# Optimization experiments

Hardware: AMD Instinct MI355X
Metric: run time of the kernel (lower is better)

## Reference

```python
import jax, jax.numpy as jnp
import numpy as np

G, M, H, HEADS, FFN, MAX_DIST, E = 8, 1024, 256, 8, 1024, 5, 131072
N = G * M
HD = H // HEADS

def _ln(x, g, b, eps=1e-5):
    m = x.mean(-1, keepdims=True)
    v = ((x - m) ** 2).mean(-1, keepdims=True)
    return (x - m) / jnp.sqrt(v + eps) * g + b

def _forward(x, gcn_w, gcn_b, qkv_w, qkv_b, proj_w, proj_b,
             ln1_g, ln1_b, ln2_g, ln2_b, ffn1_w, ffn1_b, ffn2_w, ffn2_b,
             bias_emb, oln1_g, oln1_b, oln2_g, oln2_b,
             offn1_w, offn1_b, offn2_w, offn2_b, edge_index, batch):
    src, dst = edge_index[0], edge_index[1]
    # --- local conv: GCNConv (self-loops + symmetric normalization) ---
    sl = jnp.arange(N, dtype=src.dtype)
    s2 = jnp.concatenate([src, sl]); d2 = jnp.concatenate([dst, sl])
    xw = x @ gcn_w.T
    deg = jax.ops.segment_sum(jnp.ones_like(d2, dtype=x.dtype), d2, num_segments=N)
    dinv = jnp.where(deg > 0, 1.0 / jnp.sqrt(deg), 0.0)
    norm = dinv[s2] * dinv[d2]
    x_local = jax.ops.segment_sum(xw[s2] * norm[:, None], d2, num_segments=N) + gcn_b
    # --- to_dense_batch ---
    counts = jax.ops.segment_sum(jnp.ones(N, jnp.int32), batch, num_segments=G)
    starts = jnp.concatenate([jnp.zeros(1, jnp.int32), jnp.cumsum(counts)[:-1]])
    local = jnp.arange(N, dtype=jnp.int32) - starts[batch]
    dense_x = jnp.zeros((G, M, H), x.dtype).at[batch, local].set(x)
    mask = jnp.zeros((G, M), bool).at[batch, local].set(True)
    # --- SPD via batched boolean adjacency powering (== per-node BFS capped at MAX_DIST) ---
    g_e = batch[src]
    valid = (batch[src] == batch[dst]) & (src != dst)
    ls, ld = local[src], local[dst]
    adj = jnp.zeros((G, M, M), bool).at[g_e, ls, ld].max(valid).at[g_e, ld, ls].max(valid)
    dist = jnp.full((G, M, M), MAX_DIST + 1, jnp.int32)
    eye = jnp.eye(M, dtype=bool)[None]
    dist = jnp.where(eye & mask[:, :, None], 0, dist)
    reach = adj
    dist = jnp.where(reach, jnp.minimum(dist, 1), dist)
    for d in range(2, MAX_DIST + 1):
        reach = jnp.einsum('gij,gjk->gik', reach.astype(x.dtype), adj.astype(x.dtype)) > 0
        dist = jnp.where(reach, jnp.minimum(dist, d), dist)
    attn_bias = bias_emb[dist][..., 0]  # [G, M, M]
    # --- Graphormer encoder layer (layers=1) ---
    h = dense_x
    qkv = (h @ qkv_w.T + qkv_b).reshape(G, M, 3, HEADS, HD).transpose(2, 0, 3, 1, 4)
    q, k, v = qkv[0], qkv[1], qkv[2]  # [G, heads, M, hd]
    scores = jnp.einsum('ghqd,ghkd->ghqk', q, k) * (HD ** -0.5)
    scores = scores + attn_bias[:, None].astype(scores.dtype)
    pad = ~mask
    scores = jnp.where(pad[:, None, None, :], -jnp.inf, scores)
    attn = jax.nn.softmax(scores, axis=-1)
    out = jnp.einsum('ghqk,ghkd->ghqd', attn, v).transpose(0, 2, 1, 3).reshape(G, M, H)
    out = out @ proj_w.T + proj_b
    h = _ln(h + out, ln1_g, ln1_b)
    ff = jax.nn.gelu(h @ ffn1_w.T + ffn1_b, approximate=False) @ ffn2_w.T + ffn2_b
    h = _ln(h + ff, ln2_g, ln2_b)
    h = jnp.where(pad[..., None], 0.0, h)
    x_global = h[batch, local]
    # --- GPS combine + outer FFN (dropout = identity at eval) ---
    y = _ln(x + (x_local + x_global), oln1_g, oln1_b)
    ff2 = jax.nn.gelu(y @ offn1_w.T + offn1_b, approximate=False) @ offn2_w.T + offn2_b
    return _ln(y + ff2, oln2_g, oln2_b)

def setup_inputs() -> dict:
    key = jax.random.key(0)
    ks = jax.random.split(key, 16)
    w = lambda k, *s: jax.random.normal(k, s, jnp.float32) * 0.02
    src = jax.random.randint(ks[0], (E,), 0, N, jnp.int32)
    # keep each edge inside one graph (graphs are contiguous blocks of M nodes)
    dst = (src // M) * M + jax.random.randint(ks[1], (E,), 0, M, jnp.int32)
    return dict(
        x=jax.random.normal(ks[2], (N, H), jnp.float32),
        gcn_w=w(ks[3], H, H), gcn_b=jnp.zeros((H,), jnp.float32),
        qkv_w=w(ks[4], 3 * H, H), qkv_b=jnp.zeros((3 * H,), jnp.float32),
        proj_w=w(ks[5], H, H), proj_b=jnp.zeros((H,), jnp.float32),
        ln1_g=jnp.ones((H,), jnp.float32), ln1_b=jnp.zeros((H,), jnp.float32),
        ln2_g=jnp.ones((H,), jnp.float32), ln2_b=jnp.zeros((H,), jnp.float32),
        ffn1_w=w(ks[6], FFN, H), ffn1_b=jnp.zeros((FFN,), jnp.float32),
        ffn2_w=w(ks[7], H, FFN), ffn2_b=jnp.zeros((H,), jnp.float32),
        bias_emb=w(ks[8], MAX_DIST + 2, 1),
        oln1_g=jnp.ones((H,), jnp.float32), oln1_b=jnp.zeros((H,), jnp.float32),
        oln2_g=jnp.ones((H,), jnp.float32), oln2_b=jnp.zeros((H,), jnp.float32),
        offn1_w=w(ks[9], FFN, H), offn1_b=jnp.zeros((FFN,), jnp.float32),
        offn2_w=w(ks[10], H, FFN), offn2_b=jnp.zeros((H,), jnp.float32),
        edge_index=jnp.stack([src, dst]),
        batch=(jnp.arange(N, dtype=jnp.int32) // M),
    )

def reference(x, gcn_w, gcn_b, qkv_w, qkv_b, proj_w, proj_b,
              ln1_g, ln1_b, ln2_g, ln2_b, ffn1_w, ffn1_b, ffn2_w, ffn2_b,
              bias_emb, oln1_g, oln1_b, oln2_g, oln2_b,
              offn1_w, offn1_b, offn2_w, offn2_b, edge_index, batch):
    return _forward(x, gcn_w, gcn_b, qkv_w, qkv_b, proj_w, proj_b,
                    ln1_g, ln1_b, ln2_g, ln2_b, ffn1_w, ffn1_b, ffn2_w, ffn2_b,
                    bias_emb, oln1_g, oln1_b, oln2_g, oln2_b,
                    offn1_w, offn1_b, offn2_w, offn2_b, edge_index, batch)
```

## Files before the change

### kernel.cpp

```cpp
#include <hip/hip_runtime.h>
#include <hip/hip_bf16.h>
#include <cstdint>

#define G 8
#define M 1024
#define H 256
#define HEADS 8
#define FFND 1024
#define NE 131072
#define NN (G*M)
#define HD 32

typedef unsigned long long u64;
typedef uint8_t u8;
typedef unsigned short ushort_t;
typedef __attribute__((ext_vector_type(8))) short bf16x8;
typedef __attribute__((ext_vector_type(4))) float f32x4;

__device__ __forceinline__ short f2b(float v) {
  __hip_bfloat16 h = __float2bfloat16(v);
  return *reinterpret_cast<short*>(&h);
}
__device__ __forceinline__ float b2f(unsigned int u) {
  union { float f; unsigned int i; } v; v.i = u << 16; return v.f;
}

typedef __attribute__((address_space(1))) const void gvoid;
typedef __attribute__((address_space(3))) void lvoid;
__device__ __forceinline__ void gload16(const void* g, void* l) {
  __builtin_amdgcn_global_load_lds((gvoid*)g, (lvoid*)l, 16, 0, 0);
}

__global__ void k_prep(const int* __restrict__ srcv, const int* __restrict__ dstv,
                       int* __restrict__ deg, int* __restrict__ deg2) {
  int e = blockIdx.x * 256 + threadIdx.x;
  if (e >= NE) return;
  int d = dstv[e], s = srcv[e];
  atomicAdd(&deg[d], 1);
  if (s != d) { atomicAdd(&deg2[s], 1); atomicAdd(&deg2[d], 1); }
}

__global__ __launch_bounds__(1024) void k_scan2(const int* __restrict__ deg, const int* __restrict__ deg2,
                                                int* __restrict__ starts, int* __restrict__ starts2,
                                                float* __restrict__ dinv) {
  __shared__ int tmp[1024];
  const int* in = blockIdx.x ? deg2 : deg;
  int* outp = blockIdx.x ? starts2 : starts;
  int t = threadIdx.x;
  int base = t * 8;
  int v[8]; int s = 0;
  #pragma unroll
  for (int i = 0; i < 8; ++i) { v[i] = in[base + i]; s += v[i]; }
  if (blockIdx.x == 0) {
    #pragma unroll
    for (int i = 0; i < 8; ++i) dinv[base + i] = rsqrtf((float)(v[i] + 1));
  }
  tmp[t] = s;
  __syncthreads();
  for (int off = 1; off < 1024; off <<= 1) {
    int x = (t >= off) ? tmp[t - off] : 0;
    __syncthreads();
    tmp[t] += x;
    __syncthreads();
  }
  int ex = (t == 0) ? 0 : tmp[t - 1];
  #pragma unroll
  for (int i = 0; i < 8; ++i) { outp[base + i] = ex; ex += v[i]; }
}

__global__ void k_fillb(const int* __restrict__ srcv, const int* __restrict__ dstv,
                        const int* __restrict__ starts, int* __restrict__ cursor,
                        int* __restrict__ csr,
                        const int* __restrict__ starts2, int* __restrict__ cur2,
                        int* __restrict__ nbr) {
  int e = blockIdx.x * 256 + threadIdx.x;
  if (e >= NE) return;
  int d = dstv[e], s = srcv[e];
  int pos = atomicAdd(&cursor[d], 1);
  csr[starts[d] + pos] = s;
  if (s != d) {
    int p = atomicAdd(&cur2[s], 1); nbr[starts2[s] + p] = d;
    p = atomicAdd(&cur2[d], 1);     nbr[starts2[d] + p] = s;
  }
}

__global__ __launch_bounds__(256) void k_gather(const int* __restrict__ csr,
    const int* __restrict__ starts, const int* __restrict__ deg,
    const float* __restrict__ dinv, const ushort_t* __restrict__ xwb,
    const float* __restrict__ gcn_b, float* __restrict__ xloc) {
  int d = blockIdx.x, t = threadIdx.x;
  int s0 = starts[d], cnt = deg[d];
  float acc = 0.f;
  for (int j = 0; j < cnt; ++j) {
    int s = csr[s0 + j];
    acc += dinv[s] * b2f(xwb[(size_t)s * H + t]);
  }
  float di = dinv[d];
  float self = b2f(xwb[(size_t)d * H + t]);
  xloc[(size_t)d * H + t] = di * acc + di * di * self + gcn_b[t];
}

__global__ __launch_bounds__(1024) void k_spdm(const int* __restrict__ starts2,
                                               const int* __restrict__ deg2,
                                               const int* __restrict__ nbr,
                                               u8* __restrict__ dist) {
  __shared__ unsigned int Abuf[1024], Bbuf[1024];
  __shared__ u8 dtile[1024][32];
  const int g = blockIdx.x >> 5, w = blockIdx.x & 31;
  const int i = threadIdx.x;
  const int gi = (g << 10) | i;
  unsigned int self = ((i >> 5) == w) ? (1u << (i & 31)) : 0u;
  Abuf[i] = self;
  uint4 six; six.x = six.y = six.z = six.w = 0x06060606u;
  *reinterpret_cast<uint4*>(&dtile[i][0])  = six;
  *reinterpret_cast<uint4*>(&dtile[i][16]) = six;
  if (self) dtile[i][i & 31] = 0;
  const int s0 = starts2[gi], cnt = deg2[gi];
  unsigned int* prev = Abuf;
  unsigned int* cur  = Bbuf;
  unsigned int vis = self;
  __syncthreads();
  for (int l = 1; l <= 5; ++l) {
    unsigned int acc = vis;
    for (int e = 0; e < cnt; ++e)
      acc |= prev[nbr[s0 + e] & 1023];
    unsigned int newly = acc & ~vis;
    while (newly) {
      int k = __ffs(newly) - 1;
      newly &= newly - 1;
      dtile[i][k] = (u8)l;
    }
    cur[i] = acc;
    vis = acc;
    __syncthreads();
    unsigned int* tsw = prev; prev = cur; cur = tsw;
  }
  u8* drow = dist + ((size_t)gi << 10) + w * 32;
  *reinterpret_cast<uint4*>(drow)      = *reinterpret_cast<const uint4*>(&dtile[i][0]);
  *reinterpret_cast<uint4*>(drow + 16) = *reinterpret_cast<const uint4*>(&dtile[i][16]);
}

#define WB_GCN   0
#define WB_QKV   65536
#define WB_PROJ  262144
#define WB_FFN1  327680
#define WB_FFN2  589824
#define WB_OFFN1 851968
#define WB_OFFN2 1114112
#define WB_TOTAL 1376256
#define NXBLK 2048
#define NWBLK 5376

__global__ void k_cvtall(const float* __restrict__ x,
                         const float* p0, const float* p1, const float* p2,
                         const float* p3, const float* p4, const float* p5, const float* p6,
                         const float* __restrict__ qkv_b,
                         ushort_t* __restrict__ x_bf, ushort_t* __restrict__ w_bf,
                         float* __restrict__ bias_cat) {
  int bid = blockIdx.x, t = threadIdx.x;
  if (bid < NXBLK) {
    int i = bid * 256 + t;
    float4 v = reinterpret_cast<const float4*>(x)[i];
    unsigned int lo = (unsigned int)(ushort_t)f2b(v.x) | ((unsigned int)(ushort_t)f2b(v.y) << 16);
    unsigned int hi = (unsigned int)(ushort_t)f2b(v.z) | ((unsigned int)(ushort_t)f2b(v.w) << 16);
    reinterpret_cast<uint2*>(x_bf)[i] = make_uint2(lo, hi);
  } else if (bid < NXBLK + NWBLK) {
    int i = (bid - NXBLK) * 256 + t;
    const float* src; int off;
    if (i < WB_QKV)        { src = p0; off = i; }
    else if (i < WB_PROJ)  { src = p1; off = i - WB_QKV; }
    else if (i < WB_FFN1)  { src = p2; off = i - WB_PROJ; }
    else if (i < WB_FFN2)  { src = p3; off = i - WB_FFN1; }
    else if (i < WB_OFFN1) { src = p4; off = i - WB_FFN2; }
    else if (i < WB_OFFN2) { src = p5; off = i - WB_OFFN1; }
    else                   { src = p6; off = i - WB_OFFN2; }
    w_bf[i] = (ushort_t)f2b(src[off]);
  } else {
    for (int i = t; i < 1024; i += 256) bias_cat[i] = (i < 256) ? 0.f : qkv_b[i - 256];
  }
}

template<int BM, int ACT, int OMODE>
__global__ __launch_bounds__(256) void k_mgemm(const short* __restrict__ A,
                                               const short* __restrict__ W,
                                               const float* __restrict__ bias,
                                               float* __restrict__ Cf,
                                               short* __restrict__ Cb,
                                               short* __restrict__ Cb2,
                                               int K, int O) {
  constexpr int FM = BM / 32;
  __shared__ __attribute__((aligned(16))) short As[BM * 64];
  __shared__ __attribute__((aligned(16))) short Ws[64 * 64];
  const int tid = threadIdx.x;
  const int lane = tid & 63, wbase = tid & 192;
  const int wid = tid >> 6;
  const int lg = lane >> 4, lr = lane & 15;
  const int wm = wid >> 1, wn = wid & 1;
  const int m0 = blockIdx.y * BM, n0 = blockIdx.x * 64;
  f32x4 acc[FM][2];
  #pragma unroll
  for (int i = 0; i < FM; ++i)
    #pragma unroll
    for (int j = 0; j < 2; ++j)
      acc[i][j] = (f32x4){0.f, 0.f, 0.f, 0.f};

  for (int k0 = 0; k0 < K; k0 += 64) {
    #pragma unroll
    for (int c = 0; c < BM / 32; ++c) {
      int chunk = c * 256 + tid;
      int row = chunk >> 3, ks = chunk & 7;
      int srcks = ks ^ (row & 7);
      gload16(A + (size_t)(m0 + row) * K + k0 + srcks * 8,
              (char*)As + (c * 256 + wbase) * 16);
    }
    #pragma unroll
    for (int c = 0; c < 2; ++c) {
      int chunk = c * 256 + tid;
      int row = chunk >> 3, ks = chunk & 7;
      int srcks = ks ^ (row & 7);
      gload16(W + (size_t)(n0 + row) * K + k0 + srcks * 8,
              (char*)Ws + (c * 256 + wbase) * 16);
    }
    __syncthreads();
    #pragma unroll
    for (int kk = 0; kk < 2; ++kk) {
      const int d = kk * 4 + lg;
      bf16x8 b[2];
      #pragma unroll
      for (int fn = 0; fn < 2; ++fn) {
        int r = wn * 32 + fn * 16 + lr;
        b[fn] = *reinterpret_cast<const bf16x8*>((const char*)Ws + r * 128 + ((d ^ (r & 7)) * 16));
      }
      #pragma unroll
      for (int fm = 0; fm < FM; ++fm) {
        int r = wm * (BM / 2) + fm * 16 + lr;
        bf16x8 a = *reinterpret_cast<const bf16x8*>((const char*)As + r * 128 + ((d ^ (r & 7)) * 16));
        acc[fm][0] = __builtin_amdgcn_mfma_f32_16x16x32_bf16(a, b[0], acc[fm][0], 0, 0, 0);
        acc[fm][1] = __builtin_amdgcn_mfma_f32_16x16x32_bf16(a, b[1], acc[fm][1], 0, 0, 0);
      }
    }
    __syncthreads();
  }
  #pragma unroll
  for (int fm = 0; fm < FM; ++fm)
    #pragma unroll
    for (int fn = 0; fn < 2; ++fn)
      #pragma unroll
      for (int rg = 0; rg < 4; ++rg) {
        int r = m0 + wm * (BM / 2) + fm * 16 + lg * 4 + rg;
        int cc = n0 + wn * 32 + fn * 16 + lr;
        float v = acc[fm][fn][rg] + (bias ? bias[cc] : 0.f);
        if (ACT == 1) v = 0.5f * v * (1.0f + erff(v * 0.70710678118654752f));
        if (OMODE == 0) Cf[(size_t)r * O + cc] = v;
        else if (OMODE == 1) Cb[(size_t)r * O + cc] = f2b(v);
        else {
          if (cc < 256) Cb2[(size_t)r * 256 + cc] = f2b(v);
          else          Cb[(size_t)r * 768 + cc - 256] = f2b(v);
        }
      }
}

__global__ __launch_bounds__(256) void k_attn(const ushort_t* __restrict__ qkv,
                                              const u8* __restrict__ dist,
                                              const float* __restrict__ emb,
                                              short* __restrict__ attno) {
  __shared__ __attribute__((aligned(16))) char KsB[64 * 80];
  __shared__ __attribute__((aligned(16))) char VtB[32 * 128 + 64];
  __shared__ __attribute__((aligned(16))) char PB[4][16 * 128];
  __shared__ __attribute__((aligned(16))) u8 Ds[64 * 80];
  __shared__ float semb[8];
  const int g = blockIdx.z, head = blockIdx.y;
  const int q0 = blockIdx.x * 64;
  const int t = threadIdx.x, lane = t & 63, wid = t >> 6;
  const int lg = lane >> 4, lr = lane & 15;
  if (t < 7) semb[t] = emb[t] * 1.44269504088896341f;
  const size_t nodebase = (size_t)(g * M) * 768;
  const float C1 = 0.17677669529663687f * 1.44269504088896341f;

  bf16x8 qfrag = *reinterpret_cast<const bf16x8*>(
      qkv + nodebase + (size_t)(q0 + wid * 16 + lr) * 768 + head * 32 + lg * 8);

  const int srow = t >> 2, sc = t & 3;
  uint4 kr, vr, dr;
  {
    size_t kn = nodebase + (size_t)(srow) * 768 + head * 32;
    kr = *reinterpret_cast<const uint4*>(qkv + kn + 256 + sc * 8);
    vr = *reinterpret_cast<const uint4*>(qkv + kn + 512 + sc * 8);
    dr = *reinterpret_cast<const uint4*>(dist + (size_t)(g * M + srow) * M + q0 + sc * 16);
  }

  f32x4 o0 = {0.f, 0.f, 0.f, 0.f}, o1 = {0.f, 0.f, 0.f, 0.f};
  float lpart[4] = {0.f, 0.f, 0.f, 0.f};
  char* pb = PB[wid];
  const int kp = srow >> 1;
  const int odd = srow & 1;
  const int d0 = sc * 8;

  for (int kt = 0; kt < 16; ++kt) {
    *reinterpret_cast<uint4*>(KsB + srow * 80 + sc * 16) = kr;
    *reinterpret_cast<uint4*>(Ds + srow * 80 + sc * 16) = dr;
    {
      uint4 pvr;
      pvr.x = (unsigned int)__shfl_xor((int)vr.x, 4);
      pvr.y = (unsigned int)__shfl_xor((int)vr.y, 4);
      pvr.z = (unsigned int)__shfl_xor((int)vr.z, 4);
      pvr.w = (unsigned int)__shfl_xor((int)vr.w, 4);
      unsigned int ev[4], ov[4];
      ev[0] = odd ? pvr.x : vr.x; ev[1] = odd ? pvr.y : vr.y;
      ev[2] = odd ? pvr.z : vr.z; ev[3] = odd ? pvr.w : vr.w;
      ov[0] = odd ? vr.x : pvr.x; ov[1] = odd ? vr.y : pvr.y;
      ov[2] = odd ? vr.z : pvr.z; ov[3] = odd ? vr.w : pvr.w;
      #pragma unroll
      for (int di = 0; di < 4; ++di) {
        int dd = odd * 4 + di;
        int d = d0 + dd;
        unsigned int e16 = (dd & 1) ? (ev[dd >> 1] >> 16) : (ev[dd >> 1] & 0xffff);
        unsigned int o16 = (dd & 1) ? (ov[dd >> 1] >> 16) : (ov[dd >> 1] & 0xffff);
        *reinterpret_cast<unsigned int*>(VtB + d * 128 + ((d >> 3) << 4) + ((kp << 2) ^ ((d & 7) << 4)))
            = e16 | (o16 << 16);
      }
    }
    __syncthreads();

    {
      int ktn = (kt + 1) & 15;
      size_t kn = nodebase + (size_t)(ktn * 64 + srow) * 768 + head * 32;
      kr = *reinterpret_cast<const uint4*>(qkv + kn + 256 + sc * 8);
      vr = *reinterpret_cast<const uint4*>(qkv + kn + 512 + sc * 8);
      dr = *reinterpret_cast<const uint4*>(dist + (size_t)(g * M + ktn * 64 + srow) * M + q0 + sc * 16);
    }

    f32x4 s[4];
    unsigned int d4[4];
    #pragma unroll
    for (int fn = 0; fn < 4; ++fn) {
      bf16x8 b = *reinterpret_cast<const bf16x8*>(KsB + (fn * 16 + lr) * 80 + lg * 16);
      s[fn] = __builtin_amdgcn_mfma_f32_16x16x32_bf16(qfrag, b, (f32x4){0.f,0.f,0.f,0.f}, 0, 0, 0);
      d4[fn] = *reinterpret_cast<const unsigned int*>(Ds + (fn * 16 + lr) * 80 + wid * 16 + 4 * lg);
    }
    #pragma unroll
    for (int fn = 0; fn < 4; ++fn)
      #pragma unroll
      for (int rg = 0; rg < 4; ++rg)
        s[fn][rg] = exp2f(s[fn][rg] * C1 + semb[(d4[fn] >> (8 * rg)) & 255]);
    #pragma unroll
    for (int rg = 0; rg < 4; ++rg)
      lpart[rg] += (s[0][rg] + s[1][rg]) + (s[2][rg] + s[3][rg]);

    #pragma unroll
    for (int fn = 0; fn < 4; ++fn)
      #pragma unroll
      for (int rg = 0; rg < 4; ++rg) {
        int qq = 4 * lg + rg, key = fn * 16 + lr;
        *reinterpret_cast<ushort_t*>(pb + qq * 128 + ((key * 2) ^ ((qq & 7) << 4))) =
            (ushort_t)f2b(s[fn][rg]);
      }

    #pragma unroll
    for (int kh = 0; kh < 2; ++kh) {
      int c = kh * 4 + lg;
      int chx = (c << 4) ^ ((lr & 7) << 4);
      bf16x8 a  = *reinterpret_cast<const bf16x8*>(pb + lr * 128 + chx);
      bf16x8 b0 = *reinterpret_cast<const bf16x8*>(VtB + lr * 128 + ((lr >> 3) << 4) + chx);
      bf16x8 b1 = *reinterpret_cast<const bf16x8*>(VtB + (16 + lr) * 128 + (((16 + lr) >> 3) << 4) + chx);
      o0 = __builtin_amdgcn_mfma_f32_16x16x32_bf16(a, b0, o0, 0, 0, 0);
      o1 = __builtin_amdgcn_mfma_f32_16x16x32_bf16(a, b1, o1, 0, 0, 0);
    }
    __syncthreads();
  }

  #pragma unroll
  for (int rg = 0; rg < 4; ++rg) {
    float l = lpart[rg];
    l += __shfl_xor(l, 1);
    l += __shfl_xor(l, 2);
    l += __shfl_xor(l, 4);
    l += __shfl_xor(l, 8);
    float inv = 1.0f / l;
    size_t qn = (size_t)(g * M + q0 + wid * 16 + 4 * lg + rg);
    attno[qn * H + head * 32 + lr]      = f2b(o0[rg] * inv);
    attno[qn * H + head * 32 + 16 + lr] = f2b(o1[rg] * inv);
  }
}

__global__ __launch_bounds__(256) void k_ln(const float* __restrict__ a, const float* __restrict__ b,
                                            const float* __restrict__ c3,
                                            const float* __restrict__ gam, const float* __restrict__ bet,
                                            float* __restrict__ out, ushort_t* __restrict__ outb) {
  int wid = threadIdx.x >> 6, lane = threadIdx.x & 63;
  int row = blockIdx.x * 4 + wid;
  size_t base = (size_t)row * H + lane * 4;
  float4 v = *reinterpret_cast<const float4*>(a + base);
  float4 vb = *reinterpret_cast<const float4*>(b + base);
  v.x += vb.x; v.y += vb.y; v.z += vb.z; v.w += vb.w;
  if (c3) {
    float4 vc = *reinterpret_cast<const float4*>(c3 + base);
    v.x += vc.x; v.y += vc.y; v.z += vc.z; v.w += vc.w;
  }
  float s = v.x + v.y + v.z + v.w;
  float s2 = v.x*v.x + v.y*v.y + v.z*v.z + v.w*v.w;
  #pragma unroll
  for (int off = 1; off <= 32; off <<= 1) {
    s  += __shfl_xor(s, off);
    s2 += __shfl_xor(s2, off);
  }
  float mean = s * (1.0f / 256.0f);
  float rstd = rsqrtf(s2 * (1.0f / 256.0f) - mean * mean + 1e-5f);
  float4 gg = *reinterpret_cast<const float4*>(gam + lane * 4);
  float4 bb = *reinterpret_cast<const float4*>(bet + lane * 4);
  float4 r;
  r.x = (v.x - mean) * rstd * gg.x + bb.x;
  r.y = (v.y - mean) * rstd * gg.y + bb.y;
  r.z = (v.z - mean) * rstd * gg.z + bb.z;
  r.w = (v.w - mean) * rstd * gg.w + bb.w;
  *reinterpret_cast<float4*>(out + base) = r;
  if (outb) {
    unsigned int lo = (unsigned int)(ushort_t)f2b(r.x) | ((unsigned int)(ushort_t)f2b(r.y) << 16);
    unsigned int hi = (unsigned int)(ushort_t)f2b(r.z) | ((unsigned int)(ushort_t)f2b(r.w) << 16);
    *reinterpret_cast<uint2*>(outb + base) = make_uint2(lo, hi);
  }
}

extern "C" void kernel_launch(void* const* d_in, const int* in_sizes, int n_in,
                              void* d_out, int out_size, void* d_ws, size_t ws_size,
                              hipStream_t stream) {
  const float* x      = (const float*)d_in[0];
  const float* gcn_w  = (const float*)d_in[1];
  const float* gcn_b  = (const float*)d_in[2];
  const float* qkv_w  = (const float*)d_in[3];
  const float* qkv_b  = (const float*)d_in[4];
  const float* proj_w = (const float*)d_in[5];
  const float* proj_b = (const float*)d_in[6];
  const float* ln1_g  = (const float*)d_in[7];
  const float* ln1_b  = (const float*)d_in[8];
  const float* ln2_g  = (const float*)d_in[9];
  const float* ln2_b  = (const float*)d_in[10];
  const float* ffn1_w = (const float*)d_in[11];
  const float* ffn1_b = (const float*)d_in[12];
  const float* ffn2_w = (const float*)d_in[13];
  const float* ffn2_b = (const float*)d_in[14];
  const float* bias_e = (const float*)d_in[15];
  const float* oln1_g = (const float*)d_in[16];
  const float* oln1_b = (const float*)d_in[17];
  const float* oln2_g = (const float*)d_in[18];
  const float* oln2_b = (const float*)d_in[19];
  const float* offn1_w= (const float*)d_in[20];
  const float* offn1_b= (const float*)d_in[21];
  const float* offn2_w= (const float*)d_in[22];
  const float* offn2_b= (const float*)d_in[23];
  const int*   eidx   = (const int*)d_in[24];
  const int* esrc = eidx;
  const int* edst = eidx + NE;

  char* wsp = (char*)d_ws;
  size_t off = 0;
  auto alloc = [&](size_t bytes) { void* p = wsp + off; off += (bytes + 255) & ~255ull; return p; };
  const size_t SZ_NH = (size_t)NN * H * 4;
  ushort_t* x_bf  = (ushort_t*)alloc((size_t)NN * H * 2);
  ushort_t* w_bf  = (ushort_t*)alloc((size_t)WB_TOTAL * 2);
  float* bias_cat = (float*)alloc(1024 * 4);
  ushort_t* xwb   = (ushort_t*)alloc((size_t)NN * H * 2);
  float* xloc = (float*)alloc(SZ_NH);
  float* dinv = (float*)alloc((size_t)NN * 4);
  int*   deg  = (int*)  alloc((size_t)NN * 4);
  int* cursor = (int*)  alloc((size_t)NN * 4);
  int*  deg2  = (int*)  alloc((size_t)NN * 4);
  int* cursor2= (int*)  alloc((size_t)NN * 4);
  int* starts = (int*)  alloc((size_t)NN * 4);
  int* starts2= (int*)  alloc((size_t)NN * 4);
  int*   csr  = (int*)  alloc((size_t)NE * 4);
  int*   nbr  = (int*)  alloc((size_t)2 * NE * 4);
  u8*    dist = (u8*)   alloc((size_t)NN * M);
  ushort_t* qkvb = (ushort_t*)alloc((size_t)NN * 768 * 2);
  float* h1   = (float*)alloc(SZ_NH);
  ushort_t* h1_bf = (ushort_t*)alloc((size_t)NN * H * 2);
  float* f2   = (float*)alloc(SZ_NH);
  float* h2   = (float*)alloc(SZ_NH);
  float* y    = (float*)alloc(SZ_NH);

  ushort_t* attno = x_bf;
  float* projo = h2;
  ushort_t* mid = (ushort_t*)dist;
  ushort_t* y_bf = h1_bf;
  float* outp = (float*)d_out;

  ushort_t* proj_wb = w_bf + WB_PROJ;
  ushort_t* ffn1_wb = w_bf + WB_FFN1;
  ushort_t* ffn2_wb = w_bf + WB_FFN2;
  ushort_t* offn1_wb= w_bf + WB_OFFN1;
  ushort_t* offn2_wb= w_bf + WB_OFFN2;

  hipMemsetAsync(deg, 0, (size_t)4 * NN * 4, stream);

  k_cvtall<<<NXBLK + NWBLK + 1, 256, 0, stream>>>(x, gcn_w, qkv_w, proj_w, ffn1_w,
                                                  ffn2_w, offn1_w, offn2_w, qkv_b,
                                                  x_bf, w_bf, bias_cat);

  k_prep<<<NE / 256, 256, 0, stream>>>(esrc, edst, deg, deg2);
  k_scan2<<<2, 1024, 0, stream>>>(deg, deg2, starts, starts2, dinv);
  k_fillb<<<NE / 256, 256, 0, stream>>>(esrc, edst, starts, cursor, csr, starts2, cursor2, nbr);

  k_mgemm<128, 0, 2><<<dim3(1024 / 64, NN / 128), 256, 0, stream>>>(
      (const short*)x_bf, (const short*)w_bf, bias_cat, nullptr, (short*)qkvb, (short*)xwb, 256, 1024);
  k_gather<<<NN, 256, 0, stream>>>(csr, starts, deg, dinv, xwb, gcn_b, xloc);

  k_spdm<<<G * 32, 1024, 0, stream>>>(starts2, deg2, nbr, dist);

  k_attn<<<dim3(M / 64, HEADS, G), 256, 0, stream>>>(qkvb, dist, bias_e, (short*)attno);
  k_mgemm<64, 0, 0><<<dim3(256 / 64, NN / 64), 256, 0, stream>>>(
      (const short*)attno, (const short*)proj_wb, proj_b, projo, nullptr, nullptr, 256, 256);
  k_ln<<<NN / 4, 256, 0, stream>>>(x, projo, nullptr, ln1_g, ln1_b, h1, h1_bf);
  k_mgemm<128, 1, 1><<<dim3(FFND / 64, NN / 128), 256, 0, stream>>>(
      (const short*)h1_bf, (const short*)ffn1_wb, ffn1_b, nullptr, (short*)mid, nullptr, 256, FFND);
  k_mgemm<64, 0, 0><<<dim3(256 / 64, NN / 64), 256, 0, stream>>>(
      (const short*)mid, (const short*)ffn2_wb, ffn2_b, f2, nullptr, nullptr, FFND, 256);
  k_ln<<<NN / 4, 256, 0, stream>>>(h1, f2, nullptr, ln2_g, ln2_b, h2, nullptr);

  k_ln<<<NN / 4, 256, 0, stream>>>(x, xloc, h2, oln1_g, oln1_b, y, y_bf);
  k_mgemm<128, 1, 1><<<dim3(FFND / 64, NN / 128), 256, 0, stream>>>(
      (const short*)y_bf, (const short*)offn1_wb, offn1_b, nullptr, (short*)mid, nullptr, 256, FFND);
  k_mgemm<64, 0, 0><<<dim3(256 / 64, NN / 64), 256, 0, stream>>>(
      (const short*)mid, (const short*)offn2_wb, offn2_b, f2, nullptr, nullptr, FFND, 256);
  k_ln<<<NN / 4, 256, 0, stream>>>(y, f2, nullptr, oln2_g, oln2_b, outp, nullptr);
}
```

Before: 389.7 us.

## Fuse N=256 output GEMMs with residual add and LayerNorm; swizzle attention LDS

Adds a k_gemmln kernel in which each block computes a full 32x256 output row tile. The kernel adds bias and residual, then does the LayerNorm with cross-wave reductions in the epilogue. This replaces three GEMM+LN pairs, removing the fp32 intermediate write/read and three launches. Separately, the attention kernel's K and dist LDS tiles change from padded rows to an XOR-swizzled 128-byte layout to avoid bank conflicts. The new GEMM stages the whole 256-row weight tile per block (32KB LDS) with only 256 blocks, which may reduce occupancy and reuse versus the old tiled GEMM.

```diff
diff --git a/kernel.cpp b/kernel.cpp
--- a/kernel.cpp
+++ b/kernel.cpp
@@ -184,7 +184,6 @@
 __global__ __launch_bounds__(256) void k_mgemm(const short* __restrict__ A,
                                                const short* __restrict__ W,
                                                const float* __restrict__ bias,
-                                               float* __restrict__ Cf,
                                                short* __restrict__ Cb,
                                                short* __restrict__ Cb2,
                                                int K, int O) {
@@ -251,8 +250,7 @@
         int cc = n0 + wn * 32 + fn * 16 + lr;
         float v = acc[fm][fn][rg] + (bias ? bias[cc] : 0.f);
         if (ACT == 1) v = 0.5f * v * (1.0f + erff(v * 0.70710678118654752f));
-        if (OMODE == 0) Cf[(size_t)r * O + cc] = v;
-        else if (OMODE == 1) Cb[(size_t)r * O + cc] = f2b(v);
+        if (OMODE == 1) Cb[(size_t)r * O + cc] = f2b(v);
         else {
           if (cc < 256) Cb2[(size_t)r * 256 + cc] = f2b(v);
           else          Cb[(size_t)r * 768 + cc - 256] = f2b(v);
@@ -260,14 +258,133 @@
       }
 }
 
+template<int KK, int OUTB>
+__global__ __launch_bounds__(256) void k_gemmln(const short* __restrict__ A,
+                                                const short* __restrict__ W,
+                                                const float* __restrict__ bias,
+                                                const float* __restrict__ res1,
+                                                const float* __restrict__ gam,
+                                                const float* __restrict__ bet,
+                                                float* __restrict__ outf,
+                                                ushort_t* __restrict__ outb) {
+  __shared__ __attribute__((aligned(16))) short As[32 * 64];
+  __shared__ __attribute__((aligned(16))) short Ws[256 * 64];
+  __shared__ float redS[4][32], redQ[4][32];
+  const int tid = threadIdx.x, lane = tid & 63, wid = tid >> 6;
+  const int wbase = tid & 192;
+  const int lg = lane >> 4, lr = lane & 15;
+  const int m0 = blockIdx.x * 32;
+  f32x4 acc[2][4];
+  #pragma unroll
+  for (int i = 0; i < 2; ++i)
+    #pragma unroll
+    for (int j = 0; j < 4; ++j)
+      acc[i][j] = (f32x4){0.f, 0.f, 0.f, 0.f};
+
+  for (int k0 = 0; k0 < KK; k0 += 64) {
+    {
+      int row = tid >> 3, ks = tid & 7, srcks = ks ^ (row & 7);
+      gload16(A + (size_t)(m0 + row) * KK + k0 + srcks * 8,
+              (char*)As + wbase * 16);
+    }
+    #pragma unroll
+    for (int c = 0; c < 8; ++c) {
+      int chunk = c * 256 + tid;
+      int row = chunk >> 3, ks = chunk & 7;
+      int srcks = ks ^ (row & 7);
+      gload16(W + (size_t)row * KK + k0 + srcks * 8,
+              (char*)Ws + (c * 256 + wbase) * 16);
+    }
+    __syncthreads();
+    #pragma unroll
+    for (int kk = 0; kk < 2; ++kk) {
+      const int d = kk * 4 + lg;
+      bf16x8 a[2];
+      #pragma unroll
+      for (int fr = 0; fr < 2; ++fr) {
+        int r = fr * 16 + lr;
+        a[fr] = *reinterpret_cast<const bf16x8*>((const char*)As + r * 128 + ((d ^ (r & 7)) * 16));
+      }
+      #pragma unroll
+      for (int fc = 0; fc < 4; ++fc) {
+        int r = wid * 64 + fc * 16 + lr;
+        bf16x8 b = *reinterpret_cast<const bf16x8*>((const char*)Ws + r * 128 + ((d ^ (r & 7)) * 16));
+        acc[0][fc] = __builtin_amdgcn_mfma_f32_16x16x32_bf16(a[0], b, acc[0][fc], 0, 0, 0);
+        acc[1][fc] = __builtin_amdgcn_mfma_f32_16x16x32_bf16(a[1], b, acc[1][fc], 0, 0, 0);
+      }
+    }
+    __syncthreads();
+  }
+
+  float vs[2][4][4];
+  float ps[2][4], pq[2][4];
+  #pragma unroll
+  for (int fr = 0; fr < 2; ++fr)
+    #pragma unroll
+    for (int rg = 0; rg < 4; ++rg) { ps[fr][rg] = 0.f; pq[fr][rg] = 0.f; }
+  #pragma unroll
+  for (int fc = 0; fc < 4; ++fc) {
+    int col = wid * 64 + fc * 16 + lr;
+    float bv = bias[col];
+    #pragma unroll
+    for (int fr = 0; fr < 2; ++fr)
+      #pragma unroll
+      for (int rg = 0; rg < 4; ++rg) {
+        int row = m0 + fr * 16 + 4 * lg + rg;
+        float v = acc[fr][fc][rg] + bv + res1[(size_t)row * 256 + col];
+        vs[fr][fc][rg] = v;
+        ps[fr][rg] += v; pq[fr][rg] += v * v;
+      }
+  }
+  #pragma unroll
+  for (int fr = 0; fr < 2; ++fr)
+    #pragma unroll
+    for (int rg = 0; rg < 4; ++rg) {
+      float s = ps[fr][rg], q = pq[fr][rg];
+      s += __shfl_xor(s, 1); q += __shfl_xor(q, 1);
+      s += __shfl_xor(s, 2); q += __shfl_xor(q, 2);
+      s += __shfl_xor(s, 4); q += __shfl_xor(q, 4);
+      s += __shfl_xor(s, 8); q += __shfl_xor(q, 8);
+      ps[fr][rg] = s; pq[fr][rg] = q;
+    }
+  if (lr == 0) {
+    #pragma unroll
+    for (int fr = 0; fr < 2; ++fr)
+      #pragma unroll
+      for (int rg = 0; rg < 4; ++rg) {
+        redS[wid][fr * 16 + 4 * lg + rg] = ps[fr][rg];
+        redQ[wid][fr * 16 + 4 * lg + rg] = pq[fr][rg];
+      }
+  }
+  __syncthreads();
+  #pragma unroll
+  for (int fr = 0; fr < 2; ++fr)
+    #pragma unroll
+    for (int rg = 0; rg < 4; ++rg) {
+      int rl = fr * 16 + 4 * lg + rg;
+      float S = redS[0][rl] + redS[1][rl] + redS[2][rl] + redS[3][rl];
+      float Q = redQ[0][rl] + redQ[1][rl] + redQ[2][rl] + redQ[3][rl];
+      float mean = S * (1.0f / 256.0f);
+      float rstd = rsqrtf(Q * (1.0f / 256.0f) - mean * mean + 1e-5f);
+      #pragma unroll
+      for (int fc = 0; fc < 4; ++fc) {
+        int col = wid * 64 + fc * 16 + lr;
+        float v = (vs[fr][fc][rg] - mean) * rstd * gam[col] + bet[col];
+        size_t o = (size_t)(m0 + rl) * 256 + col;
+        outf[o] = v;
+        if (OUTB) outb[o] = (ushort_t)f2b(v);
+      }
+    }
+}
+
 __global__ __launch_bounds__(256) void k_attn(const ushort_t* __restrict__ qkv,
                                               const u8* __restrict__ dist,
                                               const float* __restrict__ emb,
                                               short* __restrict__ attno) {
-  __shared__ __attribute__((aligned(16))) char KsB[64 * 80];
+  __shared__ __attribute__((aligned(16))) char KsB[32 * 128];
   __shared__ __attribute__((aligned(16))) char VtB[32 * 128 + 64];
   __shared__ __attribute__((aligned(16))) char PB[4][16 * 128];
-  __shared__ __attribute__((aligned(16))) u8 Ds[64 * 80];
+  __shared__ __attribute__((aligned(16))) u8 Ds[32 * 128];
   __shared__ float semb[8];
   const int g = blockIdx.z, head = blockIdx.y;
   const int q0 = blockIdx.x * 64;
@@ -281,6 +398,7 @@
       qkv + nodebase + (size_t)(q0 + wid * 16 + lr) * 768 + head * 32 + lg * 8);
 
   const int srow = t >> 2, sc = t & 3;
+  const int prow8 = t >> 3, pslot = (t & 7) ^ (prow8 & 7);
   uint4 kr, vr, dr;
   {
     size_t kn = nodebase + (size_t)(srow) * 768 + head * 32;
@@ -295,10 +413,17 @@
   const int kp = srow >> 1;
   const int odd = srow & 1;
   const int d0 = sc * 8;
+  int r8f[4], slK[4], slD[4];
+  #pragma unroll
+  for (int fn = 0; fn < 4; ++fn) {
+    r8f[fn] = fn * 8 + (lr >> 1);
+    slK[fn] = (((lr & 1) << 2) | lg) ^ (r8f[fn] & 7);
+    slD[fn] = (((lr & 1) << 2) | wid) ^ (r8f[fn] & 7);
+  }
 
   for (int kt = 0; kt < 16; ++kt) {
-    *reinterpret_cast<uint4*>(KsB + srow * 80 + sc * 16) = kr;
-    *reinterpret_cast<uint4*>(Ds + srow * 80 + sc * 16) = dr;
+    *reinterpret_cast<uint4*>(KsB + prow8 * 128 + pslot * 16) = kr;
+    *reinterpret_cast<uint4*>(Ds + prow8 * 128 + pslot * 16) = dr;
     {
       uint4 pvr;
       pvr.x = (unsigned int)__shfl_xor((int)vr.x, 4);
@@ -334,9 +459,9 @@
     unsigned int d4[4];
     #pragma unroll
     for (int fn = 0; fn < 4; ++fn) {
-      bf16x8 b = *reinterpret_cast<const bf16x8*>(KsB + (fn * 16 + lr) * 80 + lg * 16);
+      bf16x8 b = *reinterpret_cast<const bf16x8*>(KsB + r8f[fn] * 128 + slK[fn] * 16);
       s[fn] = __builtin_amdgcn_mfma_f32_16x16x32_bf16(qfrag, b, (f32x4){0.f,0.f,0.f,0.f}, 0, 0, 0);
-      d4[fn] = *reinterpret_cast<const unsigned int*>(Ds + (fn * 16 + lr) * 80 + wid * 16 + 4 * lg);
+      d4[fn] = *reinterpret_cast<const unsigned int*>(Ds + r8f[fn] * 128 + slD[fn] * 16 + 4 * lg);
     }
     #pragma unroll
     for (int fn = 0; fn < 4; ++fn)
@@ -474,12 +599,10 @@
   ushort_t* qkvb = (ushort_t*)alloc((size_t)NN * 768 * 2);
   float* h1   = (float*)alloc(SZ_NH);
   ushort_t* h1_bf = (ushort_t*)alloc((size_t)NN * H * 2);
-  float* f2   = (float*)alloc(SZ_NH);
   float* h2   = (float*)alloc(SZ_NH);
   float* y    = (float*)alloc(SZ_NH);
 
   ushort_t* attno = x_bf;
-  float* projo = h2;
   ushort_t* mid = (ushort_t*)dist;
   ushort_t* y_bf = h1_bf;
   float* outp = (float*)d_out;
@@ -501,25 +624,22 @@
   k_fillb<<<NE / 256, 256, 0, stream>>>(esrc, edst, starts, cursor, csr, starts2, cursor2, nbr);
 
   k_mgemm<128, 0, 2><<<dim3(1024 / 64, NN / 128), 256, 0, stream>>>(
-      (const short*)x_bf, (const short*)w_bf, bias_cat, nullptr, (short*)qkvb, (short*)xwb, 256, 1024);
+      (const short*)x_bf, (const short*)w_bf, bias_cat, (short*)qkvb, (short*)xwb, 256, 1024);
   k_gather<<<NN, 256, 0, stream>>>(csr, starts, deg, dinv, xwb, gcn_b, xloc);
 
   k_spdm<<<G * 32, 1024, 0, stream>>>(starts2, deg2, nbr, dist);
 
   k_attn<<<dim3(M / 64, HEADS, G), 256, 0, stream>>>(qkvb, dist, bias_e, (short*)attno);
-  k_mgemm<64, 0, 0><<<dim3(256 / 64, NN / 64), 256, 0, stream>>>(
-      (const short*)attno, (const short*)proj_wb, proj_b, projo, nullptr, nullptr, 256, 256);
-  k_ln<<<NN / 4, 256, 0, stream>>>(x, projo, nullptr, ln1_g, ln1_b, h1, h1_bf);
+  k_gemmln<256, 1><<<NN / 32, 256, 0, stream>>>(
+      (const short*)attno, (const short*)proj_wb, proj_b, x, ln1_g, ln1_b, h1, h1_bf);
   k_mgemm<128, 1, 1><<<dim3(FFND / 64, NN / 128), 256, 0, stream>>>(
-      (const short*)h1_bf, (const short*)ffn1_wb, ffn1_b, nullptr, (short*)mid, nullptr, 256, FFND);
-  k_mgemm<64, 0, 0><<<dim3(256 / 64, NN / 64), 256, 0, stream>>>(
-      (const short*)mid, (const short*)ffn2_wb, ffn2_b, f2, nullptr, nullptr, FFND, 256);
-  k_ln<<<NN / 4, 256, 0, stream>>>(h1, f2, nullptr, ln2_g, ln2_b, h2, nullptr);
+      (const short*)h1_bf, (const short*)ffn1_wb, ffn1_b, (short*)mid, nullptr, 256, FFND);
+  k_gemmln<1024, 0><<<NN / 32, 256, 0, stream>>>(
+      (const short*)mid, (const short*)ffn2_wb, ffn2_b, h1, ln2_g, ln2_b, h2, nullptr);
 
   k_ln<<<NN / 4, 256, 0, stream>>>(x, xloc, h2, oln1_g, oln1_b, y, y_bf);
   k_mgemm<128, 1, 1><<<dim3(FFND / 64, NN / 128), 256, 0, stream>>>(
-      (const short*)y_bf, (const short*)offn1_wb, offn1_b, nullptr, (short*)mid, nullptr, 256, FFND);
-  k_mgemm<64, 0, 0><<<dim3(256 / 64, NN / 64), 256, 0, stream>>>(
-      (const short*)mid, (const short*)offn2_wb, offn2_b, f2, nullptr, nullptr, FFND, 256);
-  k_ln<<<NN / 4, 256, 0, stream>>>(y, f2, nullptr, oln2_g, oln2_b, outp, nullptr);
-}
+      (const short*)y_bf, (const short*)offn1_wb, offn1_b, (short*)mid, nullptr, 256, FFND);
+  k_gemmln<1024, 0><<<NN / 32, 256, 0, stream>>>(
+      (const short*)mid, (const short*)offn2_wb, offn2_b, y, oln2_g, oln2_b, outp, nullptr);
+}
```

Result: faster. 374.6 us (-3.9%).
